# Kernel optimization log

Hardware: AMD Instinct MI355X
Metric: run time of the kernel (lower is better)

The kernel has to match this reference:

```python
import jax, jax.numpy as jnp
import numpy as np

ACT_BIT = 8
WEIGHT_BIT = 8
BIAS_BIT = 32
EPS = 1e-8


def _sym_scale(sat_max, bit):
    # symmetric_linear_quantization_params: scale = clamp(sat, 1e-8) / (2^(b-1)-1)
    n = 2 ** (bit - 1) - 1
    return jnp.maximum(sat_max, EPS) / n


def _sym_quant(x, scale, bit):
    # SymmetricQuantFunction: round(x/scale) clamped to [-2^(b-1), 2^(b-1)-1]
    n = 2 ** (bit - 1) - 1
    return jnp.clip(jnp.round(x / scale), -n - 1, n)


def setup_inputs() -> dict:
    key = jax.random.key(0)
    kx, kw, kb = jax.random.split(key, 3)
    B, S, D_IN, D_OUT = 4, 2048, 4096, 4096
    x = jax.random.normal(kx, (B, S, D_IN), dtype=jnp.float32)
    W = jax.random.normal(kw, (D_OUT, D_IN), dtype=jnp.float32) * 0.02
    b = jax.random.normal(kb, (D_OUT,), dtype=jnp.float32) * 0.02
    return {"x": x, "W": W, "b": b}


def reference(x, W, b):
    # --- QuantAct (per-tensor symmetric int8, min/max from x itself) ---
    x_min, x_max = x.min(), x.max()
    act_scale = _sym_scale(jnp.maximum(jnp.abs(x_min), jnp.abs(x_max)), ACT_BIT)
    x_int = _sym_quant(x, act_scale, ACT_BIT)  # [B,S,Din], int values in fp32

    # --- QuantLinearBase (per-tensor symmetric int8 weight, int32 bias) ---
    w_sat = jnp.maximum(jnp.abs(W.min()), jnp.abs(W.max()))
    w_scale = _sym_scale(w_sat, WEIGHT_BIT)
    w_int = _sym_quant(W, w_scale, WEIGHT_BIT)  # [Dout,Din]

    bias_scale = act_scale * w_scale
    n32 = 2 ** (BIAS_BIT - 1) - 1
    b_int = jnp.clip(jnp.round(b / bias_scale), -n32 - 1, n32)  # [Dout]

    # integer GEMM + bias, then rescale by act_scale * w_scale
    out_int = jnp.einsum("bsi,oi->bso", x_int, w_int) + b_int
    return out_int * bias_scale
```

## Files before the change

### kernel.cpp

```cpp
#include <hip/hip_runtime.h>
#include <cstdint>
#include <cstddef>


typedef int v4i __attribute__((ext_vector_type(4)));

__device__ __forceinline__ void async_copy16(const void* g, void* s) {
  __builtin_amdgcn_global_load_lds(
      (const __attribute__((address_space(1))) void*)g,
      (__attribute__((address_space(3))) void*)s, 16, 0, 0);
}

__device__ __forceinline__ float block_max(float m) {
  __shared__ float smax[4];
#pragma unroll
  for (int off = 32; off > 0; off >>= 1)
    m = fmaxf(m, __shfl_down(m, off, 64));
  if ((threadIdx.x & 63) == 0) smax[threadIdx.x >> 6] = m;
  __syncthreads();
  return fmaxf(fmaxf(smax[0], smax[1]), fmaxf(smax[2], smax[3]));
}

#define NBX 1024
#define NBW 512

__global__ __launch_bounds__(256) void absmax_partial_kernel(
    const float4* __restrict__ x, int xn4, const float4* __restrict__ w,
    int wn4, float* __restrict__ px, float* __restrict__ pw) {
  const float4* src;
  float* dst;
  int n4, bid, nb;
  if (blockIdx.x < NBX) {
    src = x; n4 = xn4; dst = px; bid = blockIdx.x; nb = NBX;
  } else {
    src = w; n4 = wn4; dst = pw; bid = blockIdx.x - NBX; nb = NBW;
  }
  float m = 0.0f;
  for (int i = bid * 256 + threadIdx.x; i < n4; i += nb * 256) {
    float4 v = src[i];
    m = fmaxf(m, fmaxf(fmaxf(fabsf(v.x), fabsf(v.y)),
                       fmaxf(fabsf(v.z), fabsf(v.w))));
  }
  m = block_max(m);
  if (threadIdx.x == 0) dst[bid] = m;
}

__global__ __launch_bounds__(256) void absmax_final_kernel(
    const float* __restrict__ px, const float* __restrict__ pw,
    float* __restrict__ sat) {
  const float* src = (blockIdx.x == 0) ? px : pw;
  const int n = (blockIdx.x == 0) ? NBX : NBW;
  float m = 0.0f;
  for (int i = threadIdx.x; i < n; i += 256) m = fmaxf(m, src[i]);
  m = block_max(m);
  if (threadIdx.x == 0) {
    sat[blockIdx.x] = m;
    sat[2 + blockIdx.x] = 127.0f / fmaxf(m, 1e-8f);
  }
}

__device__ __forceinline__ int pack4(float4 v, float inv) {
  int a = (int)fminf(fmaxf(rintf(v.x * inv), -128.0f), 127.0f);
  int b = (int)fminf(fmaxf(rintf(v.y * inv), -128.0f), 127.0f);
  int c = (int)fminf(fmaxf(rintf(v.z * inv), -128.0f), 127.0f);
  int d = (int)fminf(fmaxf(rintf(v.w * inv), -128.0f), 127.0f);
  return (a & 255) | ((b & 255) << 8) | ((c & 255) << 16) | ((d & 255) << 24);
}

#define QNB 2048

__global__ __launch_bounds__(256) void quant_fused_kernel(
    const float4* __restrict__ x, int xn16, const float4* __restrict__ w,
    int wn16, const float* __restrict__ sat, int4* __restrict__ xq,
    int4* __restrict__ wq) {
  const float invx = sat[2];
  const float invw = sat[3];
  const int nth = QNB * 256;
  const int t = blockIdx.x * 256 + threadIdx.x;
  for (int u = t; u < xn16; u += nth) {
    const float4* p = x + (size_t)u * 4;
    int4 o;
    o.x = pack4(p[0], invx);
    o.y = pack4(p[1], invx);
    o.z = pack4(p[2], invx);
    o.w = pack4(p[3], invx);
    xq[u] = o;
  }
  for (int u = t; u < wn16; u += nth) {
    const float4* p = w + (size_t)u * 4;
    int4 o;
    o.x = pack4(p[0], invw);
    o.y = pack4(p[1], invw);
    o.z = pack4(p[2], invw);
    o.w = pack4(p[3], invw);
    wq[u] = o;
  }
}

__global__ __launch_bounds__(512, 2) void i8_gemm_kernel(
    const signed char* __restrict__ Aq, const signed char* __restrict__ Bq,
    const float* __restrict__ bias, const float* __restrict__ sat,
    float* __restrict__ out, int M, int N, int K) {
  __shared__ signed char lds[4][2][256 * 64];

  const int tid = threadIdx.x;
  const int lane = tid & 63;
  const int wid = tid >> 6;
  const int wr = wid >> 2;
  const int wc = wid & 3;
  const int r15 = lane & 15;
  const int q4 = lane >> 4;

  const int nwg = gridDim.x * gridDim.y;
  int bid = blockIdx.y * gridDim.x + blockIdx.x;
  if ((nwg & 7) == 0) bid = (bid & 7) * (nwg >> 3) + (bid >> 3);
  const int N0 = (bid % gridDim.x) * 256;
  const int M0 = (bid / gridDim.x) * 256;

  const int srow = tid >> 2;
  const int sb = tid & 3;
  const int cg = (sb - ((srow >> 1) & 3)) & 3;
  const signed char* Ag = Aq + (size_t)(M0 + srow) * K + cg * 16;
  const signed char* Bg = Bq + (size_t)(N0 + srow) * K + cg * 16;
  const int d0 = srow * 64 + sb * 16;
  const size_t rstep = (size_t)128 * K;

  const int kboff = ((q4 + ((r15 >> 1) & 3)) & 3) * 16;

  v4i acc[8][4] = {};
  const int nt = K >> 6;

  for (int T = 0; T < 3; ++T) {
    const size_t ko = (size_t)T << 6;
    signed char* bA = &lds[T & 3][0][0];
    signed char* bB = &lds[T & 3][1][0];
    async_copy16(Ag + ko, bA + d0);
    async_copy16(Ag + ko + rstep, bA + d0 + 8192);
    async_copy16(Bg + ko, bB + d0);
    async_copy16(Bg + ko + rstep, bB + d0 + 8192);
  }
  asm volatile("s_waitcnt vmcnt(8)" ::: "memory");
  __builtin_amdgcn_s_barrier();

  for (int t = 0; t < nt; ++t) {
    const signed char* bA = &lds[t & 3][0][0];
    const signed char* bB = &lds[t & 3][1][0];
    const int tp = t + 3;
    const bool st = tp < nt;
    signed char* sA = &lds[tp & 3][0][0];
    signed char* sB = &lds[tp & 3][1][0];
    const size_t ko = (size_t)tp << 6;

    v4i af[4], bf[4];

#pragma unroll
    for (int f = 0; f < 4; ++f) {
      af[f] = *(const v4i*)(bA + (wr * 128 + f * 16 + r15) * 64 + kboff);
      bf[f] = *(const v4i*)(bB + (wc * 64 + f * 16 + r15) * 64 + kboff);
    }
    if (st) {
      async_copy16(Ag + ko, sA + d0);
      async_copy16(Ag + ko + rstep, sA + d0 + 8192);
    }
    __builtin_amdgcn_s_barrier();
    asm volatile("s_waitcnt lgkmcnt(0)" ::: "memory");
    __builtin_amdgcn_sched_barrier(0);
    __builtin_amdgcn_s_setprio(1);
#pragma unroll
    for (int fm = 0; fm < 4; ++fm)
#pragma unroll
      for (int fn = 0; fn < 4; ++fn)
        acc[fm][fn] = __builtin_amdgcn_mfma_i32_16x16x64_i8(
            af[fm], bf[fn], acc[fm][fn], 0, 0, 0);
    __builtin_amdgcn_s_setprio(0);
    __builtin_amdgcn_s_barrier();

#pragma unroll
    for (int f = 0; f < 4; ++f) {
      af[f] = *(const v4i*)(bA + (wr * 128 + 64 + f * 16 + r15) * 64 + kboff);
    }
    if (st) {
      async_copy16(Bg + ko, sB + d0);
      async_copy16(Bg + ko + rstep, sB + d0 + 8192);
    }
    __builtin_amdgcn_s_barrier();
    asm volatile("s_waitcnt lgkmcnt(0)" ::: "memory");
    __builtin_amdgcn_sched_barrier(0);
    __builtin_amdgcn_s_setprio(1);
#pragma unroll
    for (int fm = 0; fm < 4; ++fm)
#pragma unroll
      for (int fn = 0; fn < 4; ++fn)
        acc[4 + fm][fn] = __builtin_amdgcn_mfma_i32_16x16x64_i8(
            af[fm], bf[fn], acc[4 + fm][fn], 0, 0, 0);
    __builtin_amdgcn_s_setprio(0);
    if (t < nt - 3) {
      asm volatile("s_waitcnt vmcnt(8)" ::: "memory");
    } else if (t == nt - 3) {
      asm volatile("s_waitcnt vmcnt(4)" ::: "memory");
    } else if (t == nt - 2) {
      asm volatile("s_waitcnt vmcnt(0)" ::: "memory");
    }
    __builtin_amdgcn_s_barrier();
  }

  const float act_s = fmaxf(sat[0], 1e-8f) / 127.0f;
  const float w_s = fmaxf(sat[1], 1e-8f) / 127.0f;
  const float bscale = act_s * w_s;

#pragma unroll
  for (int fn = 0; fn < 4; ++fn) {
    const int col = N0 + wc * 64 + fn * 16 + r15;
    const float fb = rintf(bias[col] / bscale);
#pragma unroll
    for (int f = 0; f < 8; ++f) {
      const int row0 = M0 + wr * 128 + f * 16 + q4 * 4;
#pragma unroll
      for (int rr = 0; rr < 4; ++rr) {
        out[(size_t)(row0 + rr) * N + col] =
            ((float)acc[f][fn][rr] + fb) * bscale;
      }
    }
  }
}

extern "C" void kernel_launch(void* const* d_in, const int* in_sizes, int n_in,
                              void* d_out, int out_size, void* d_ws,
                              size_t ws_size, hipStream_t stream) {
  const float* x = (const float*)d_in[0];
  const float* W = (const float*)d_in[1];
  const float* b = (const float*)d_in[2];
  float* out = (float*)d_out;

  const int Dout = in_sizes[2];
  const int K = in_sizes[1] / Dout;
  const int M = in_sizes[0] / K;
  const int N = Dout;

  float* sat = (float*)d_ws;
  float* px = sat + 16;
  float* pw = px + NBX;
  signed char* xq = (signed char*)d_ws + 8192;
  signed char* wq = xq + (size_t)M * K;

  const int xn4 = in_sizes[0] / 4;
  const int wn4 = in_sizes[1] / 4;

  absmax_partial_kernel<<<NBX + NBW, 256, 0, stream>>>(
      (const float4*)x, xn4, (const float4*)W, wn4, px, pw);
  absmax_final_kernel<<<2, 256, 0, stream>>>(px, pw, sat);
  quant_fused_kernel<<<QNB, 256, 0, stream>>>(
      (const float4*)x, xn4 / 4, (const float4*)W, wn4 / 4, sat, (int4*)xq,
      (int4*)wq);

  dim3 grid(N / 256, M / 256);
  i8_gemm_kernel<<<grid, 512, 0, stream>>>(xq, wq, b, sat, out, M, N, K);
}
```

Before: 438.2 us.

## Fuse absmax finalize into quant, unroll GEMM K-loop, vectorize epilogue via LDS

Removes the separate absmax_final kernel launch: every quant block now reduces the partial maxima itself and block 0 writes the saturation values. The GEMM main loop is manually unrolled by four with compile-time buffer indices, which avoids per-iteration modulo indexing. The epilogue stages the accumulators through LDS so each lane writes contiguous float4 rows using nontemporal stores, replacing scattered scalar stores. The cost is redundant partial-max reduction in every quant block, plus larger code size.

```diff
diff --git a/kernel.cpp b/kernel.cpp
--- a/kernel.cpp
+++ b/kernel.cpp
@@ -4,6 +4,7 @@
 
 
 typedef int v4i __attribute__((ext_vector_type(4)));
+typedef float v4f __attribute__((ext_vector_type(4)));
 
 __device__ __forceinline__ void async_copy16(const void* g, void* s) {
   __builtin_amdgcn_global_load_lds(
@@ -45,20 +46,6 @@
   if (threadIdx.x == 0) dst[bid] = m;
 }
 
-__global__ __launch_bounds__(256) void absmax_final_kernel(
-    const float* __restrict__ px, const float* __restrict__ pw,
-    float* __restrict__ sat) {
-  const float* src = (blockIdx.x == 0) ? px : pw;
-  const int n = (blockIdx.x == 0) ? NBX : NBW;
-  float m = 0.0f;
-  for (int i = threadIdx.x; i < n; i += 256) m = fmaxf(m, src[i]);
-  m = block_max(m);
-  if (threadIdx.x == 0) {
-    sat[blockIdx.x] = m;
-    sat[2 + blockIdx.x] = 127.0f / fmaxf(m, 1e-8f);
-  }
-}
-
 __device__ __forceinline__ int pack4(float4 v, float inv) {
   int a = (int)fminf(fmaxf(rintf(v.x * inv), -128.0f), 127.0f);
   int b = (int)fminf(fmaxf(rintf(v.y * inv), -128.0f), 127.0f);
@@ -71,10 +58,21 @@
 
 __global__ __launch_bounds__(256) void quant_fused_kernel(
     const float4* __restrict__ x, int xn16, const float4* __restrict__ w,
-    int wn16, const float* __restrict__ sat, int4* __restrict__ xq,
-    int4* __restrict__ wq) {
-  const float invx = sat[2];
-  const float invw = sat[3];
+    int wn16, const float* __restrict__ px, const float* __restrict__ pw,
+    float* __restrict__ sat, int4* __restrict__ xq, int4* __restrict__ wq) {
+  float mx = 0.0f, mw = 0.0f;
+  for (int i = threadIdx.x; i < NBX; i += 256) mx = fmaxf(mx, px[i]);
+  mx = block_max(mx);
+  __syncthreads();
+  for (int i = threadIdx.x; i < NBW; i += 256) mw = fmaxf(mw, pw[i]);
+  mw = block_max(mw);
+  if (blockIdx.x == 0 && threadIdx.x == 0) {
+    sat[0] = mx;
+    sat[1] = mw;
+  }
+  const float invx = 127.0f / fmaxf(mx, 1e-8f);
+  const float invw = 127.0f / fmaxf(mw, 1e-8f);
+
   const int nth = QNB * 256;
   const int t = blockIdx.x * 256 + threadIdx.x;
   for (int u = t; u < xn16; u += nth) {
@@ -97,6 +95,59 @@
   }
 }
 
+#define GEMM_KTILE(CB, SB, T, ST, VMSEL)                                       \
+  do {                                                                         \
+    const signed char* bA_ = &lds[CB][0][0];                                   \
+    const signed char* bB_ = &lds[CB][1][0];                                   \
+    signed char* sA_ = &lds[SB][0][0];                                         \
+    signed char* sB_ = &lds[SB][1][0];                                         \
+    const size_t ko_ = (size_t)((T) + 3) << 6;                                 \
+    v4i af_[4], bf_[4];                                                        \
+    _Pragma("unroll") for (int f = 0; f < 4; ++f) {                            \
+      af_[f] = *(const v4i*)(bA_ + (wr * 128 + f * 16 + r15) * 64 + kboff);    \
+      bf_[f] = *(const v4i*)(bB_ + (wc * 64 + f * 16 + r15) * 64 + kboff);     \
+    }                                                                          \
+    if (ST) {                                                                  \
+      async_copy16(Ag + ko_, sA_ + d0);                                        \
+      async_copy16(Ag + ko_ + rstep, sA_ + d0 + 8192);                         \
+    }                                                                          \
+    __builtin_amdgcn_s_barrier();                                              \
+    asm volatile("s_waitcnt lgkmcnt(0)" ::: "memory");                         \
+    __builtin_amdgcn_sched_barrier(0);                                         \
+    __builtin_amdgcn_s_setprio(1);                                             \
+    _Pragma("unroll") for (int fm = 0; fm < 4; ++fm)                           \
+        _Pragma("unroll") for (int fn = 0; fn < 4; ++fn) acc[fm][fn] =         \
+        __builtin_amdgcn_mfma_i32_16x16x64_i8(af_[fm], bf_[fn], acc[fm][fn],   \
+                                              0, 0, 0);                        \
+    __builtin_amdgcn_s_setprio(0);                                             \
+    __builtin_amdgcn_s_barrier();                                              \
+    _Pragma("unroll") for (int f = 0; f < 4; ++f) {                            \
+      af_[f] =                                                                 \
+          *(const v4i*)(bA_ + (wr * 128 + 64 + f * 16 + r15) * 64 + kboff);    \
+    }                                                                          \
+    if (ST) {                                                                  \
+      async_copy16(Bg + ko_, sB_ + d0);                                        \
+      async_copy16(Bg + ko_ + rstep, sB_ + d0 + 8192);                         \
+    }                                                                          \
+    __builtin_amdgcn_s_barrier();                                              \
+    asm volatile("s_waitcnt lgkmcnt(0)" ::: "memory");                         \
+    __builtin_amdgcn_sched_barrier(0);                                         \
+    __builtin_amdgcn_s_setprio(1);                                             \
+    _Pragma("unroll") for (int fm = 0; fm < 4; ++fm)                           \
+        _Pragma("unroll") for (int fn = 0; fn < 4; ++fn) acc[4 + fm][fn] =     \
+        __builtin_amdgcn_mfma_i32_16x16x64_i8(af_[fm], bf_[fn],                \
+                                              acc[4 + fm][fn], 0, 0, 0);       \
+    __builtin_amdgcn_s_setprio(0);                                             \
+    if ((VMSEL) == 0) {                                                        \
+      asm volatile("s_waitcnt vmcnt(8)" ::: "memory");                         \
+    } else if ((VMSEL) == 1) {                                                 \
+      asm volatile("s_waitcnt vmcnt(4)" ::: "memory");                         \
+    } else if ((VMSEL) == 2) {                                                 \
+      asm volatile("s_waitcnt vmcnt(0)" ::: "memory");                         \
+    }                                                                          \
+    __builtin_amdgcn_s_barrier();                                              \
+  } while (0)
+
 __global__ __launch_bounds__(512, 2) void i8_gemm_kernel(
     const signed char* __restrict__ Aq, const signed char* __restrict__ Bq,
     const float* __restrict__ bias, const float* __restrict__ sat,
@@ -142,84 +193,51 @@
   asm volatile("s_waitcnt vmcnt(8)" ::: "memory");
   __builtin_amdgcn_s_barrier();
 
-  for (int t = 0; t < nt; ++t) {
-    const signed char* bA = &lds[t & 3][0][0];
-    const signed char* bB = &lds[t & 3][1][0];
-    const int tp = t + 3;
-    const bool st = tp < nt;
-    signed char* sA = &lds[tp & 3][0][0];
-    signed char* sB = &lds[tp & 3][1][0];
-    const size_t ko = (size_t)tp << 6;
-
-    v4i af[4], bf[4];
-
-#pragma unroll
-    for (int f = 0; f < 4; ++f) {
-      af[f] = *(const v4i*)(bA + (wr * 128 + f * 16 + r15) * 64 + kboff);
-      bf[f] = *(const v4i*)(bB + (wc * 64 + f * 16 + r15) * 64 + kboff);
-    }
-    if (st) {
-      async_copy16(Ag + ko, sA + d0);
-      async_copy16(Ag + ko + rstep, sA + d0 + 8192);
-    }
-    __builtin_amdgcn_s_barrier();
-    asm volatile("s_waitcnt lgkmcnt(0)" ::: "memory");
-    __builtin_amdgcn_sched_barrier(0);
-    __builtin_amdgcn_s_setprio(1);
-#pragma unroll
-    for (int fm = 0; fm < 4; ++fm)
-#pragma unroll
-      for (int fn = 0; fn < 4; ++fn)
-        acc[fm][fn] = __builtin_amdgcn_mfma_i32_16x16x64_i8(
-            af[fm], bf[fn], acc[fm][fn], 0, 0, 0);
-    __builtin_amdgcn_s_setprio(0);
-    __builtin_amdgcn_s_barrier();
-
-#pragma unroll
-    for (int f = 0; f < 4; ++f) {
-      af[f] = *(const v4i*)(bA + (wr * 128 + 64 + f * 16 + r15) * 64 + kboff);
-    }
-    if (st) {
-      async_copy16(Bg + ko, sB + d0);
-      async_copy16(Bg + ko + rstep, sB + d0 + 8192);
-    }
-    __builtin_amdgcn_s_barrier();
-    asm volatile("s_waitcnt lgkmcnt(0)" ::: "memory");
-    __builtin_amdgcn_sched_barrier(0);
-    __builtin_amdgcn_s_setprio(1);
-#pragma unroll
-    for (int fm = 0; fm < 4; ++fm)
-#pragma unroll
-      for (int fn = 0; fn < 4; ++fn)
-        acc[4 + fm][fn] = __builtin_amdgcn_mfma_i32_16x16x64_i8(
-            af[fm], bf[fn], acc[4 + fm][fn], 0, 0, 0);
-    __builtin_amdgcn_s_setprio(0);
-    if (t < nt - 3) {
-      asm volatile("s_waitcnt vmcnt(8)" ::: "memory");
-    } else if (t == nt - 3) {
-      asm volatile("s_waitcnt vmcnt(4)" ::: "memory");
-    } else if (t == nt - 2) {
-      asm volatile("s_waitcnt vmcnt(0)" ::: "memory");
-    }
-    __builtin_amdgcn_s_barrier();
+  int t = 0;
+  for (; t + 7 < nt; t += 4) {
+    GEMM_KTILE(0, 3, t + 0, true, 0);
+    GEMM_KTILE(1, 0, t + 1, true, 0);
+    GEMM_KTILE(2, 1, t + 2, true, 0);
+    GEMM_KTILE(3, 2, t + 3, true, 0);
+  }
+  for (; t < nt; ++t) {
+    const int cb = t & 3;
+    const int sbuf = (t + 3) & 3;
+    const bool st = (t + 3) < nt;
+    const int vmsel =
+        (t < nt - 3) ? 0 : (t == nt - 3) ? 1 : (t == nt - 2) ? 2 : 3;
+    GEMM_KTILE(cb, sbuf, t, st, vmsel);
   }
 
   const float act_s = fmaxf(sat[0], 1e-8f) / 127.0f;
   const float w_s = fmaxf(sat[1], 1e-8f) / 127.0f;
   const float bscale = act_s * w_s;
 
-#pragma unroll
-  for (int fn = 0; fn < 4; ++fn) {
-    const int col = N0 + wc * 64 + fn * 16 + r15;
-    const float fb = rintf(bias[col] / bscale);
-#pragma unroll
-    for (int f = 0; f < 8; ++f) {
-      const int row0 = M0 + wr * 128 + f * 16 + q4 * 4;
-#pragma unroll
-      for (int rr = 0; rr < 4; ++rr) {
-        out[(size_t)(row0 + rr) * N + col] =
-            ((float)acc[f][fn][rr] + fb) * bscale;
-      }
+  float* scratch = (float*)&lds[0][0][0] + wid * 4096;
+  const float4 b4 = *(const float4*)&bias[N0 + wc * 64 + 4 * r15];
+  v4f fb4;
+  fb4.x = rintf(b4.x / bscale);
+  fb4.y = rintf(b4.y / bscale);
+  fb4.z = rintf(b4.z / bscale);
+  fb4.w = rintf(b4.w / bscale);
+
+#pragma unroll
+  for (int g = 0; g < 2; ++g) {
+#pragma unroll
+    for (int f4 = 0; f4 < 4; ++f4)
+#pragma unroll
+      for (int fn = 0; fn < 4; ++fn)
+#pragma unroll
+        for (int rr = 0; rr < 4; ++rr)
+          scratch[(f4 * 16 + q4 * 4 + rr) * 64 + fn * 16 + r15] =
+              (float)acc[g * 4 + f4][fn][rr];
+#pragma unroll
+    for (int rq = 0; rq < 16; ++rq) {
+      v4f v = *(v4f*)&scratch[(rq * 4 + q4) * 64 + 4 * r15];
+      v4f o = (v + fb4) * bscale;
+      const int row = M0 + wr * 128 + g * 64 + rq * 4 + q4;
+      __builtin_nontemporal_store(
+          o, (v4f*)&out[(size_t)row * N + N0 + wc * 64 + 4 * r15]);
     }
   }
 }
@@ -248,10 +266,9 @@
 
   absmax_partial_kernel<<<NBX + NBW, 256, 0, stream>>>(
       (const float4*)x, xn4, (const float4*)W, wn4, px, pw);
-  absmax_final_kernel<<<2, 256, 0, stream>>>(px, pw, sat);
   quant_fused_kernel<<<QNB, 256, 0, stream>>>(
-      (const float4*)x, xn4 / 4, (const float4*)W, wn4 / 4, sat, (int4*)xq,
-      (int4*)wq);
+      (const float4*)x, xn4 / 4, (const float4*)W, wn4 / 4, px, pw, sat,
+      (int4*)xq, (int4*)wq);
 
   dim3 grid(N / 256, M / 256);
   i8_gemm_kernel<<<grid, 512, 0, stream>>>(xq, wq, b, sat, out, M, N, K);
```

Result: faster. 413.1 us (-5.7%).
